# Performance work log

Measured on AMD Instinct MI355X. Metric: run time of the kernel, lower is better.

The kernel has to match this reference:

```python
import jax, jax.numpy as jnp
import numpy as np

N, C, H, W = 4, 256, 64, 64
K, G, PAD, STRIDE, DIL = 3, 8, 1, 1, 1
GC = C // G      # channels per group
P = K * K        # sampling points per group
HIN, WIN = H + 2 * PAD, W + 2 * PAD
BN_EPS = 1e-5
LN_EPS = 1e-5


def setup_inputs():
    key = jax.random.key(0)
    ks = jax.random.split(key, 8)
    f32 = jnp.float32
    return {
        "x": jax.random.normal(ks[0], (N, C, H, W), dtype=f32),
        "w_in": jax.random.normal(ks[1], (C, C), dtype=f32) * 0.05,
        "b_in": jnp.zeros((C,), f32),
        "w_dw": jax.random.normal(ks[2], (C, 1, K, K), dtype=f32) * 0.1,
        "b_dw": jnp.zeros((C,), f32),
        "ln_g": jnp.ones((C,), f32), "ln_b": jnp.zeros((C,), f32),
        "w_off": jax.random.normal(ks[3], (C, G * P * 2), dtype=f32) * 0.01,
        "b_off": jax.random.normal(ks[4], (G * P * 2,), dtype=f32) * 0.01,
        "w_mask": jax.random.normal(ks[5], (C, G * P), dtype=f32) * 0.01,
        "b_mask": jnp.zeros((G * P,), f32),
        "w_out": jax.random.normal(ks[6], (C, C), dtype=f32) * 0.05,
        "b_out": jnp.zeros((C,), f32),
        "bn_g": jnp.ones((C,), f32), "bn_b": jnp.zeros((C,), f32),
        "bn_mean": jnp.zeros((C,), f32), "bn_var": jnp.ones((C,), f32),
    }


def _bilinear(img, grid):
    # img: (B, Cc, Hh, Ww); grid: (B, S, P, 2) normalized to [-1,1],
    # matches F.grid_sample(mode='bilinear', padding_mode='zeros', align_corners=False)
    B, Cc, Hh, Ww = img.shape
    gx = (grid[..., 0] + 1.0) * 0.5 * Ww - 0.5
    gy = (grid[..., 1] + 1.0) * 0.5 * Hh - 0.5
    x0 = jnp.floor(gx)
    y0 = jnp.floor(gy)
    wx = gx - x0
    wy = gy - y0
    flat = img.reshape(B, Cc, Hh * Ww)

    def tap(xi, yi, wgt):
        valid = (xi >= 0) & (xi <= Ww - 1) & (yi >= 0) & (yi <= Hh - 1)
        idx = (jnp.clip(yi, 0, Hh - 1) * Ww + jnp.clip(xi, 0, Ww - 1)).astype(jnp.int32)
        v = jax.vmap(lambda im, ix: im[:, ix])(flat, idx)   # (B, Cc, S, P)
        return v * (wgt * valid.astype(img.dtype))[:, None]

    return (tap(x0, y0, (1 - wx) * (1 - wy)) + tap(x0 + 1, y0, wx * (1 - wy))
            + tap(x0, y0 + 1, (1 - wx) * wy) + tap(x0 + 1, y0 + 1, wx * wy))


def _forward(x, w_in, b_in, w_dw, b_dw, ln_g, ln_b, w_off, b_off,
             w_mask, b_mask, w_out, b_out, bn_g, bn_b, bn_mean, bn_var):
    xl = jnp.transpose(x, (0, 2, 3, 1))                      # (N,H,W,C) channels-last
    x_proj = xl @ w_in + b_in                                # input_proj
    # depthwise conv + LayerNorm + GELU feature branch for offset/mask prediction
    dw = jax.lax.conv_general_dilated(
        x, w_dw, (1, 1), ((PAD, PAD), (PAD, PAD)),
        feature_group_count=C, dimension_numbers=("NCHW", "OIHW", "NCHW"))
    dw = jnp.transpose(dw + b_dw[None, :, None, None], (0, 2, 3, 1))
    mu = dw.mean(-1, keepdims=True)
    var = ((dw - mu) ** 2).mean(-1, keepdims=True)
    dw = (dw - mu) * jax.lax.rsqrt(var + LN_EPS) * ln_g + ln_b
    x1 = jax.nn.gelu(dw, approximate=False)
    offset = x1 @ w_off + b_off                              # (N,H,W,G*P*2)
    mask = jax.nn.softmax((x1 @ w_mask + b_mask).reshape(N, H, W, G, P), axis=-1)
    # reference points + dilation kernel grid, normalized to padded input, (x,y) order
    ry = ((DIL * (K - 1)) // 2 + 0.5 + jnp.arange(H, dtype=x.dtype) * STRIDE) / HIN
    rx = ((DIL * (K - 1)) // 2 + 0.5 + jnp.arange(W, dtype=x.dtype) * STRIDE) / WIN
    ref = jnp.stack(jnp.broadcast_arrays(rx[None, :], ry[:, None]), axis=-1)  # (H,W,2)
    px = (jnp.arange(K, dtype=x.dtype) * DIL - (DIL * (K - 1)) // 2) / WIN
    py = (jnp.arange(K, dtype=x.dtype) * DIL - (DIL * (K - 1)) // 2) / HIN
    gx, gy = jnp.meshgrid(px, py, indexing="ij")             # kw-major flattening as in DCNv3
    kgrid = jnp.stack([gx, gy], -1).reshape(P, 2)
    norm = jnp.array([WIN, HIN], dtype=x.dtype)
    loc = (ref[None, :, :, None, None, :] + kgrid[None, None, None, None, :, :]
           + offset.reshape(N, H, W, G, P, 2) / norm)        # (N,H,W,G,P,2), offset_scale=1
    sgrid = 2.0 * loc - 1.0
    # group-split padded value tensor and deformable sampling
    xp = jnp.pad(x_proj, ((0, 0), (PAD, PAD), (PAD, PAD), (0, 0)))
    img = jnp.transpose(xp, (0, 3, 1, 2)).reshape(N * G, GC, HIN, WIN)
    sg = jnp.transpose(sgrid.reshape(N, H * W, G, P, 2), (0, 2, 1, 3, 4)).reshape(N * G, H * W, P, 2)
    sampled = _bilinear(img, sg)                             # (N*G, GC, H*W, P)
    m = jnp.transpose(mask.reshape(N, H * W, G, P), (0, 2, 1, 3)).reshape(N * G, 1, H * W, P)
    agg = (sampled * m).sum(-1)                              # (N*G, GC, H*W)
    y = jnp.transpose(agg.reshape(N, C, H * W), (0, 2, 1)).reshape(N, H, W, C)
    y = y @ w_out + b_out                                    # output_proj
    y = jnp.transpose(y, (0, 3, 1, 2))                       # back to NCHW
    y = (y - bn_mean[None, :, None, None]) * jax.lax.rsqrt(bn_var + BN_EPS)[None, :, None, None]
    y = y * bn_g[None, :, None, None] + bn_b[None, :, None, None]
    return y * jax.nn.sigmoid(y)                             # SiLU (Conv.default_act)


def reference(x, w_in, b_in, w_dw, b_dw, ln_g, ln_b, w_off, b_off,
              w_mask, b_mask, w_out, b_out, bn_g, bn_b, bn_mean, bn_var):
    return _forward(x, w_in, b_in, w_dw, b_dw, ln_g, ln_b, w_off, b_off,
                    w_mask, b_mask, w_out, b_out, bn_g, bn_b, bn_mean, bn_var)
```

## Files before the change

kernel.cpp:

```cpp
#include <hip/hip_runtime.h>
#include <math.h>

#define NB   4
#define CCH  256
#define HH   64
#define WW   64
#define GG   8
#define GCH  32
#define PP   9
#define HIN  66
#define WIN  66
#define HWSZ 4096
#define NPIX 16384

#define X16_ELEMS  (NPIX*CCH)
#define XP_ELEMS   (NB*HIN*WIN*CCH)
#define X1_ELEMS   (NPIX*CCH)
#define AGG_ELEMS  (NPIX*CCH)
#define WINT_ELEMS (CCH*CCH)
#define WOUTT_ELEMS (CCH*CCH)
#define WOMT_ELEMS (216*CCH)
#define OFF_ELEMS  (NPIX*144)
#define MSK_ELEMS  (NPIX*72)

typedef __attribute__((ext_vector_type(8))) short bf16x8;
typedef __attribute__((ext_vector_type(4))) float f32x4;

__device__ __forceinline__ unsigned short f2bf(float f) {
    unsigned int u = __float_as_uint(f);
    unsigned int r = (u + 0x7FFFu + ((u >> 16) & 1u)) >> 16;
    return (unsigned short)r;
}
__device__ __forceinline__ float bf2f(unsigned short s) {
    return __uint_as_float(((unsigned int)s) << 16);
}

#define SDW_STRIDE 258

__global__ __launch_bounds__(512) void k_dw_prep(
    const float* __restrict__ x, const float* __restrict__ w_dw,
    const float* __restrict__ b_dw, const float* __restrict__ ln_g,
    const float* __restrict__ ln_b, const float* __restrict__ w_in,
    const float* __restrict__ w_off, const float* __restrict__ w_mask,
    const float* __restrict__ w_out, unsigned short* __restrict__ x1,
    unsigned short* __restrict__ x16, unsigned short* __restrict__ win_t,
    unsigned short* __restrict__ womt, unsigned short* __restrict__ wout_t,
    unsigned short* __restrict__ xp)
{
    const int b = blockIdx.x;
    const int tid = threadIdx.x;

    if (b >= 256) {
        const int gtid = (b - 256) * 512 + tid;
        const int STRIDE = 68 * 512;
        for (int i = gtid; i < 252928; i += STRIDE) {
            if (i < 65536) {
                int n = i & 255, k = i >> 8;
                win_t[n * 256 + k] = f2bf(w_in[i]);
            } else if (i < 131072) {
                int j = i - 65536;
                int n = j & 255, k = j >> 8;
                wout_t[n * 256 + k] = f2bf(w_out[j]);
            } else if (i < 186368) {
                int j = i - 131072;
                int k = j / 216, col = j - k * 216;
                float v = (col < 144) ? w_off[k * 144 + col]
                                      : w_mask[k * 72 + col - 144];
                womt[col * 256 + k] = f2bf(v);
            } else {
                int r = i - 186368;
                int seg = r >> 6, ln = r & 63;
                int n = seg / 260, rp = seg % 260;
                int h, w;
                if (rp < 66)       { h = 0;        w = rp; }
                else if (rp < 132) { h = 65;       w = rp - 66; }
                else if (rp < 196) { h = rp - 131; w = 0; }
                else               { h = rp - 195; w = 65; }
                uint2 z = make_uint2(0u, 0u);
                *(uint2*)&xp[(((size_t)n * HIN + h) * WIN + w) * CCH + ln * 4] = z;
            }
        }
        return;
    }

    __shared__ unsigned short sdw[64 * SDW_STRIDE];
    __shared__ unsigned short sxr[64 * SDW_STRIDE];
    __shared__ float r1s[8][64];
    __shared__ float r2s[8][64];
    __shared__ float mu_s[64];
    __shared__ float rs_s[64];

    const int h = b & 63;
    const int n = b >> 6;
    const int wave = tid >> 6;
    const int lane = tid & 63;

    const float* xn = x + (size_t)n * CCH * HWSZ;
    const bool h0ok = (h > 0);
    const bool h2ok = (h < HH - 1);

    float s1 = 0.f, s2 = 0.f;

#pragma unroll 4
    for (int it = 0; it < 32; it++) {
        const int c = it * 8 + wave;
        const float* xc = xn + (size_t)c * HWSZ + h * WW + lane;
        float v0 = h0ok ? xc[-WW] : 0.f;
        float v1 = xc[0];
        float v2 = h2ok ? xc[WW] : 0.f;

        const float* wk = w_dw + c * 9;
        float acc = b_dw[c];

        float l0 = __shfl_up(v0, 1);   if (lane == 0)  l0 = 0.f;
        float r0 = __shfl_down(v0, 1); if (lane == 63) r0 = 0.f;
        acc += wk[0] * l0 + wk[1] * v0 + wk[2] * r0;

        float l1 = __shfl_up(v1, 1);   if (lane == 0)  l1 = 0.f;
        float r1 = __shfl_down(v1, 1); if (lane == 63) r1 = 0.f;
        acc += wk[3] * l1 + wk[4] * v1 + wk[5] * r1;

        float l2 = __shfl_up(v2, 1);   if (lane == 0)  l2 = 0.f;
        float r2 = __shfl_down(v2, 1); if (lane == 63) r2 = 0.f;
        acc += wk[6] * l2 + wk[7] * v2 + wk[8] * r2;

        s1 += acc;
        s2 += acc * acc;
        sdw[lane * SDW_STRIDE + c] = f2bf(acc);
        sxr[lane * SDW_STRIDE + c] = f2bf(v1);
    }

    r1s[wave][lane] = s1;
    r2s[wave][lane] = s2;
    __syncthreads();

    if (tid < 64) {
        float a1 = 0.f, a2 = 0.f;
#pragma unroll
        for (int q = 0; q < 8; q++) { a1 += r1s[q][tid]; a2 += r2s[q][tid]; }
        float mu = a1 * (1.0f / 256.0f);
        float var = a2 * (1.0f / 256.0f) - mu * mu;
        mu_s[tid] = mu;
        rs_s[tid] = rsqrtf(var + 1e-5f);
    }
    __syncthreads();

    const int c0 = (tid & 63) * 4;
    const int wq = tid >> 6;
    float g4[4], b4[4];
#pragma unroll
    for (int i = 0; i < 4; i++) { g4[i] = ln_g[c0 + i]; b4[i] = ln_b[c0 + i]; }

    unsigned short* x1p  = x1  + (((size_t)n * HH + h) * WW) * CCH + c0;
    unsigned short* x16p = x16 + (((size_t)n * HH + h) * WW) * CCH + c0;
#pragma unroll
    for (int pass = 0; pass < 8; pass++) {
        int w = wq + pass * 8;
        float mu = mu_s[w], rs = rs_s[w];
        const unsigned short* row  = &sdw[w * SDW_STRIDE + c0];
        const unsigned short* rowx = &sxr[w * SDW_STRIDE + c0];
        unsigned short tmp[4];
#pragma unroll
        for (int i = 0; i < 4; i++) {
            float v = (bf2f(row[i]) - mu) * rs * g4[i] + b4[i];
            tmp[i] = f2bf(0.5f * v * (1.0f + erff(v * 0.70710678118654752f)));
        }
        ushort4 o; o.x = tmp[0]; o.y = tmp[1]; o.z = tmp[2]; o.w = tmp[3];
        *(ushort4*)&x1p[(size_t)w * CCH] = o;
        ushort4 xo; xo.x = rowx[0]; xo.y = rowx[1]; xo.z = rowx[2]; xo.w = rowx[3];
        *(ushort4*)&x16p[(size_t)w * CCH] = xo;
    }
}

__global__ __launch_bounds__(256) void k_proj(
    const unsigned short* __restrict__ x16, const unsigned short* __restrict__ win_t,
    const float* __restrict__ b_in, unsigned short* __restrict__ xp,
    const unsigned short* __restrict__ x1, const unsigned short* __restrict__ womt,
    const float* __restrict__ b_off, const float* __restrict__ b_mask,
    float* __restrict__ off, float* __restrict__ msk)
{
    const int b = blockIdx.x;
    const int tid = threadIdx.x;
    const int wave = tid >> 6;
    const int lane = tid & 63;
    const int r16  = lane & 15;
    const int quad = lane >> 4;
    const int mw   = wave * 32;

    f32x4 acc[2][4];
#pragma unroll
    for (int i = 0; i < 2; i++)
#pragma unroll
        for (int j = 0; j < 4; j++) acc[i][j] = (f32x4){0.f, 0.f, 0.f, 0.f};

    if (b < 512) {
        const int m0  = (b & 127) * 128;
        const int co0 = (b >> 7) * 64;
        const int n   = m0 >> 12;
        const int hw0 = m0 & 4095;

        const unsigned short* a0p = x16 + (size_t)(m0 + mw + r16) * CCH + quad * 8;
        const unsigned short* a1p = a0p + 16 * CCH;

#pragma unroll
        for (int k0 = 0; k0 < CCH; k0 += 32) {
            bf16x8 a0 = *(const bf16x8*)&a0p[k0];
            bf16x8 a1 = *(const bf16x8*)&a1p[k0];
#pragma unroll
            for (int nt = 0; nt < 4; nt++) {
                bf16x8 bfr = *(const bf16x8*)&win_t[(size_t)(co0 + nt * 16 + r16) * CCH + k0 + quad * 8];
                acc[0][nt] = __builtin_amdgcn_mfma_f32_16x16x32_bf16(a0, bfr, acc[0][nt], 0, 0, 0);
                acc[1][nt] = __builtin_amdgcn_mfma_f32_16x16x32_bf16(a1, bfr, acc[1][nt], 0, 0, 0);
            }
        }

#pragma unroll
        for (int nt = 0; nt < 4; nt++) {
            int co = co0 + nt * 16 + r16;
            float bias = b_in[co];
#pragma unroll
            for (int mt = 0; mt < 2; mt++) {
                int mbase = mw + mt * 16 + quad * 4;
#pragma unroll
                for (int r = 0; r < 4; r++) {
                    int hw = hw0 + mbase + r;
                    int h = hw >> 6, w = hw & 63;
                    xp[(((size_t)n * HIN + (h + 1)) * WIN + (w + 1)) * CCH + co] =
                        f2bf(acc[mt][nt][r] + bias);
                }
            }
        }
    } else {
        const int b2 = b - 512;
        const int m0  = (b2 & 127) * 128;
        const int co0 = (b2 >> 7) * 64;

        const unsigned short* a0p = x1 + (size_t)(m0 + mw + r16) * CCH + quad * 8;
        const unsigned short* a1p = a0p + 16 * CCH;

#pragma unroll
        for (int k0 = 0; k0 < CCH; k0 += 32) {
            bf16x8 a0 = *(const bf16x8*)&a0p[k0];
            bf16x8 a1 = *(const bf16x8*)&a1p[k0];
#pragma unroll
            for (int nt = 0; nt < 4; nt++) {
                int col = co0 + nt * 16 + r16;
                int colc = (col < 216) ? col : 215;
                bf16x8 bfr = *(const bf16x8*)&womt[(size_t)colc * CCH + k0 + quad * 8];
                acc[0][nt] = __builtin_amdgcn_mfma_f32_16x16x32_bf16(a0, bfr, acc[0][nt], 0, 0, 0);
                acc[1][nt] = __builtin_amdgcn_mfma_f32_16x16x32_bf16(a1, bfr, acc[1][nt], 0, 0, 0);
            }
        }

#pragma unroll
        for (int nt = 0; nt < 4; nt++) {
            int col = co0 + nt * 16 + r16;
            if (col >= 216) continue;
            float bias = (col < 144) ? b_off[col] : b_mask[col - 144];
#pragma unroll
            for (int mt = 0; mt < 2; mt++) {
                int mbase = m0 + mw + mt * 16 + quad * 4;
#pragma unroll
                for (int r = 0; r < 4; r++) {
                    int p = mbase + r;
                    float v = acc[mt][nt][r] + bias;
                    if (col < 144) off[(size_t)p * 144 + col] = v;
                    else           msk[(size_t)p * 72 + col - 144] = v;
                }
            }
        }
    }
}

__device__ __forceinline__ void acc8_tap(float* a, uint4 vv, float wgt) {
    a[0] += wgt * __uint_as_float(vv.x << 16);
    a[1] += wgt * __uint_as_float(vv.x & 0xffff0000u);
    a[2] += wgt * __uint_as_float(vv.y << 16);
    a[3] += wgt * __uint_as_float(vv.y & 0xffff0000u);
    a[4] += wgt * __uint_as_float(vv.z << 16);
    a[5] += wgt * __uint_as_float(vv.z & 0xffff0000u);
    a[6] += wgt * __uint_as_float(vv.w << 16);
    a[7] += wgt * __uint_as_float(vv.w & 0xffff0000u);
}

__global__ __launch_bounds__(256) void k_sample_agg(
    const unsigned short* __restrict__ xp, const float* __restrict__ off,
    const float* __restrict__ msk, unsigned short* __restrict__ agg)
{
    __shared__ float  sm[576];
    __shared__ int2   tco[576];
    __shared__ float4 twt[576];

    const int tid = threadIdx.x;
    const int s0 = blockIdx.x * 8;

    if (tid < 64) {
        const int pix = tid >> 3, g = tid & 7;
        const float* mskp = msk + (size_t)(s0 + pix) * 72 + g * 9;
        float e[9];
        float mx = -1e30f;
#pragma unroll
        for (int p = 0; p < PP; p++) { e[p] = mskp[p]; mx = fmaxf(mx, e[p]); }
        float sum = 0.f;
#pragma unroll
        for (int p = 0; p < PP; p++) { e[p] = __expf(e[p] - mx); sum += e[p]; }
        float rs = 1.0f / sum;
#pragma unroll
        for (int p = 0; p < PP; p++) sm[tid * 9 + p] = e[p] * rs;
    }
    __syncthreads();

    for (int idx = tid; idx < 576; idx += 256) {
        int pix = idx / 72;
        int rem = idx - pix * 72;
        int g = rem / 9;
        int p = rem - g * 9;
        int s = s0 + pix;
        int hw = s & 4095;
        int h = hw >> 6, w = hw & 63;
        const float* offp = off + (size_t)s * 144 + g * 18 + p * 2;
        float ox = offp[0], oy = offp[1];
        int i = p / 3, j = p - i * 3;
        float fx = (float)(w + i) + ox;
        float fy = (float)(h + j) + oy;
        float x0f = floorf(fx), y0f = floorf(fy);
        int x0 = (int)x0f, y0 = (int)y0f;
        float wx = fx - x0f, wy = fy - y0f;
        float m = sm[idx];
        float w00 = (1.f - wx) * (1.f - wy) * m;
        float w10 = wx * (1.f - wy) * m;
        float w01 = (1.f - wx) * wy * m;
        float w11 = wx * wy * m;
        int x1c = x0 + 1, y1c = y0 + 1;
        if (!((x0  >= 0) && (x0  < WIN))) { w00 = 0.f; w01 = 0.f; }
        if (!((x1c >= 0) && (x1c < WIN))) { w10 = 0.f; w11 = 0.f; }
        if (!((y0  >= 0) && (y0  < HIN))) { w00 = 0.f; w10 = 0.f; }
        if (!((y1c >= 0) && (y1c < HIN))) { w01 = 0.f; w11 = 0.f; }
        int cx0 = min(max(x0, 0), WIN - 1), cx1 = min(max(x1c, 0), WIN - 1);
        int cy0 = min(max(y0, 0), HIN - 1), cy1 = min(max(y1c, 0), HIN - 1);
        tco[idx] = make_int2(cx0 | (cx1 << 16), cy0 | (cy1 << 16));
        twt[idx] = make_float4(w00, w10, w01, w11);
    }
    __syncthreads();

    const int pix = tid >> 5;
    const int l5 = tid & 31;
    const int g = l5 >> 2, c8 = l5 & 3;
    const int s = s0 + pix;
    const int n = s >> 12;
    const unsigned short* base = xp + (size_t)n * HIN * WIN * CCH + g * GCH + c8 * 8;
    const int tbase = pix * 72 + g * 9;

    float a[8];
#pragma unroll
    for (int i = 0; i < 8; i++) a[i] = 0.f;

#pragma unroll
    for (int p = 0; p < PP; p++) {
        int2 cc = tco[tbase + p];
        float4 wt = twt[tbase + p];
        int cx0 = cc.x & 0xFFFF, cx1 = cc.x >> 16;
        int cy0 = cc.y & 0xFFFF, cy1 = cc.y >> 16;
        const unsigned short* r0 = base + (size_t)(cy0 * WIN) * CCH;
        const unsigned short* r1 = base + (size_t)(cy1 * WIN) * CCH;
        uint4 v00 = *(const uint4*)&r0[(size_t)cx0 * CCH];
        uint4 v10 = *(const uint4*)&r0[(size_t)cx1 * CCH];
        uint4 v01 = *(const uint4*)&r1[(size_t)cx0 * CCH];
        uint4 v11 = *(const uint4*)&r1[(size_t)cx1 * CCH];
        acc8_tap(a, v00, wt.x);
        acc8_tap(a, v10, wt.y);
        acc8_tap(a, v01, wt.z);
        acc8_tap(a, v11, wt.w);
    }

    uint4 o;
    o.x = (unsigned int)f2bf(a[0]) | ((unsigned int)f2bf(a[1]) << 16);
    o.y = (unsigned int)f2bf(a[2]) | ((unsigned int)f2bf(a[3]) << 16);
    o.z = (unsigned int)f2bf(a[4]) | ((unsigned int)f2bf(a[5]) << 16);
    o.w = (unsigned int)f2bf(a[6]) | ((unsigned int)f2bf(a[7]) << 16);
    *(uint4*)&agg[(size_t)s * CCH + g * GCH + c8 * 8] = o;
}

__global__ __launch_bounds__(256) void k_gemm_out(
    const unsigned short* __restrict__ agg, const unsigned short* __restrict__ wout_t,
    const float* __restrict__ b_out, const float* __restrict__ bn_g,
    const float* __restrict__ bn_b, const float* __restrict__ bn_mean,
    const float* __restrict__ bn_var, float* __restrict__ out)
{
    const int m0  = blockIdx.x * 128;
    const int co0 = blockIdx.y * 64;
    const int tid = threadIdx.x;
    const int n   = m0 >> 12;
    const int hw0 = m0 & 4095;

    const int wave = tid >> 6;
    const int lane = tid & 63;
    const int r16  = lane & 15;
    const int quad = lane >> 4;
    const int mw   = wave * 32;

    f32x4 acc[2][4];
#pragma unroll
    for (int i = 0; i < 2; i++)
#pragma unroll
        for (int j = 0; j < 4; j++) acc[i][j] = (f32x4){0.f, 0.f, 0.f, 0.f};

    const unsigned short* a0p = agg + (size_t)(m0 + mw + r16) * CCH + quad * 8;
    const unsigned short* a1p = a0p + 16 * CCH;

#pragma unroll
    for (int k0 = 0; k0 < CCH; k0 += 32) {
        bf16x8 a0 = *(const bf16x8*)&a0p[k0];
        bf16x8 a1 = *(const bf16x8*)&a1p[k0];
#pragma unroll
        for (int nt = 0; nt < 4; nt++) {
            bf16x8 bfr = *(const bf16x8*)&wout_t[(size_t)(co0 + nt * 16 + r16) * CCH + k0 + quad * 8];
            acc[0][nt] = __builtin_amdgcn_mfma_f32_16x16x32_bf16(a0, bfr, acc[0][nt], 0, 0, 0);
            acc[1][nt] = __builtin_amdgcn_mfma_f32_16x16x32_bf16(a1, bfr, acc[1][nt], 0, 0, 0);
        }
    }

#pragma unroll
    for (int nt = 0; nt < 4; nt++) {
        int co = co0 + nt * 16 + r16;
        float mean = bn_mean[co];
        float rstd = rsqrtf(bn_var[co] + 1e-5f);
        float gg = bn_g[co], bb = bn_b[co], bo = b_out[co];
#pragma unroll
        for (int mt = 0; mt < 2; mt++) {
            int hwb = hw0 + mw + mt * 16 + quad * 4;
            float tmp[4];
#pragma unroll
            for (int r = 0; r < 4; r++) {
                float y = acc[mt][nt][r] + bo;
                float yh = (y - mean) * rstd * gg + bb;
                tmp[r] = yh / (1.0f + __expf(-yh));
            }
            float4 v = make_float4(tmp[0], tmp[1], tmp[2], tmp[3]);
            *(float4*)&out[((size_t)n * CCH + co) * HWSZ + hwb] = v;
        }
    }
}

extern "C" void kernel_launch(void* const* d_in, const int* in_sizes, int n_in,
                              void* d_out, int out_size, void* d_ws, size_t ws_size,
                              hipStream_t stream)
{
    const float* x       = (const float*)d_in[0];
    const float* w_in    = (const float*)d_in[1];
    const float* b_in    = (const float*)d_in[2];
    const float* w_dw    = (const float*)d_in[3];
    const float* b_dw    = (const float*)d_in[4];
    const float* ln_g    = (const float*)d_in[5];
    const float* ln_b    = (const float*)d_in[6];
    const float* w_off   = (const float*)d_in[7];
    const float* b_off   = (const float*)d_in[8];
    const float* w_mask  = (const float*)d_in[9];
    const float* b_mask  = (const float*)d_in[10];
    const float* w_out   = (const float*)d_in[11];
    const float* b_out   = (const float*)d_in[12];
    const float* bn_g    = (const float*)d_in[13];
    const float* bn_b    = (const float*)d_in[14];
    const float* bn_mean = (const float*)d_in[15];
    const float* bn_var  = (const float*)d_in[16];
    float* out = (float*)d_out;

    unsigned short* xp     = (unsigned short*)d_ws;
    unsigned short* x16    = xp + XP_ELEMS;
    unsigned short* x1     = x16 + X16_ELEMS;
    unsigned short* agg    = x1 + X1_ELEMS;
    unsigned short* win_t  = agg + AGG_ELEMS;
    unsigned short* wout_t = win_t + WINT_ELEMS;
    unsigned short* womt   = wout_t + WOUTT_ELEMS;
    float* off = (float*)(womt + WOMT_ELEMS);
    float* msk = off + OFF_ELEMS;

    k_dw_prep<<<dim3(324), 512, 0, stream>>>(x, w_dw, b_dw, ln_g, ln_b,
                                             w_in, w_off, w_mask, w_out,
                                             x1, x16, win_t, womt, wout_t, xp);
    k_proj<<<dim3(1024), 256, 0, stream>>>(x16, win_t, b_in, xp,
                                           x1, womt, b_off, b_mask, off, msk);
    k_sample_agg<<<dim3(2048), 256, 0, stream>>>(xp, off, msk, agg);
    k_gemm_out<<<dim3(128, 4), 256, 0, stream>>>(agg, wout_t, b_out, bn_g, bn_b, bn_mean, bn_var, out);
}
```

Before: 179.2 us.

## Fuse four stage kernels into one cooperative persistent kernel with grid syncs

Merges the depthwise/LN prep, input and offset/mask projections, deformable sampling and output GEMM into a single cooperative kernel of 512 blocks separated by grid.sync(). Each block now does several work items in sequence, and the dw prep moves from 512 to 256 threads per block. The aim is to remove launch gaps and kernel-boundary drains between stages. The cost is less parallelism per stage, 68KB of static shared memory limiting occupancy, and grid-wide barrier overhead. If the cooperative launch fails, it falls back to separate kernels.

```diff
diff --git a/kernel.cpp b/kernel.cpp
--- a/kernel.cpp
+++ b/kernel.cpp
@@ -1,5 +1,8 @@
 #include <hip/hip_runtime.h>
+#include <hip/hip_cooperative_groups.h>
 #include <math.h>
+
+namespace cg = cooperative_groups;
 
 #define NB   4
 #define CCH  256
@@ -37,61 +40,21 @@
 
 #define SDW_STRIDE 258
 
-__global__ __launch_bounds__(512) void k_dw_prep(
-    const float* __restrict__ x, const float* __restrict__ w_dw,
-    const float* __restrict__ b_dw, const float* __restrict__ ln_g,
-    const float* __restrict__ ln_b, const float* __restrict__ w_in,
-    const float* __restrict__ w_off, const float* __restrict__ w_mask,
-    const float* __restrict__ w_out, unsigned short* __restrict__ x1,
-    unsigned short* __restrict__ x16, unsigned short* __restrict__ win_t,
-    unsigned short* __restrict__ womt, unsigned short* __restrict__ wout_t,
-    unsigned short* __restrict__ xp)
-{
-    const int b = blockIdx.x;
-    const int tid = threadIdx.x;
-
-    if (b >= 256) {
-        const int gtid = (b - 256) * 512 + tid;
-        const int STRIDE = 68 * 512;
-        for (int i = gtid; i < 252928; i += STRIDE) {
-            if (i < 65536) {
-                int n = i & 255, k = i >> 8;
-                win_t[n * 256 + k] = f2bf(w_in[i]);
-            } else if (i < 131072) {
-                int j = i - 65536;
-                int n = j & 255, k = j >> 8;
-                wout_t[n * 256 + k] = f2bf(w_out[j]);
-            } else if (i < 186368) {
-                int j = i - 131072;
-                int k = j / 216, col = j - k * 216;
-                float v = (col < 144) ? w_off[k * 144 + col]
-                                      : w_mask[k * 72 + col - 144];
-                womt[col * 256 + k] = f2bf(v);
-            } else {
-                int r = i - 186368;
-                int seg = r >> 6, ln = r & 63;
-                int n = seg / 260, rp = seg % 260;
-                int h, w;
-                if (rp < 66)       { h = 0;        w = rp; }
-                else if (rp < 132) { h = 65;       w = rp - 66; }
-                else if (rp < 196) { h = rp - 131; w = 0; }
-                else               { h = rp - 195; w = 65; }
-                uint2 z = make_uint2(0u, 0u);
-                *(uint2*)&xp[(((size_t)n * HIN + h) * WIN + w) * CCH + ln * 4] = z;
-            }
-        }
-        return;
-    }
-
-    __shared__ unsigned short sdw[64 * SDW_STRIDE];
-    __shared__ unsigned short sxr[64 * SDW_STRIDE];
-    __shared__ float r1s[8][64];
-    __shared__ float r2s[8][64];
-    __shared__ float mu_s[64];
-    __shared__ float rs_s[64];
-
-    const int h = b & 63;
-    const int n = b >> 6;
+__device__ void dev_dw_row(int row, int tid, unsigned char* smem,
+                           const float* __restrict__ x, const float* __restrict__ w_dw,
+                           const float* __restrict__ b_dw, const float* __restrict__ ln_g,
+                           const float* __restrict__ ln_b, unsigned short* __restrict__ x1,
+                           unsigned short* __restrict__ x16)
+{
+    unsigned short* sdw = (unsigned short*)smem;
+    unsigned short* sxr = sdw + 64 * SDW_STRIDE;
+    float* r1s  = (float*)(smem + 66048);
+    float* r2s  = (float*)(smem + 67072);
+    float* mu_s = (float*)(smem + 68096);
+    float* rs_s = (float*)(smem + 68352);
+
+    const int h = row & 63;
+    const int n = row >> 6;
     const int wave = tid >> 6;
     const int lane = tid & 63;
 
@@ -102,8 +65,8 @@
     float s1 = 0.f, s2 = 0.f;
 
 #pragma unroll 4
-    for (int it = 0; it < 32; it++) {
-        const int c = it * 8 + wave;
+    for (int it = 0; it < 64; it++) {
+        const int c = it * 4 + wave;
         const float* xc = xn + (size_t)c * HWSZ + h * WW + lane;
         float v0 = h0ok ? xc[-WW] : 0.f;
         float v1 = xc[0];
@@ -130,14 +93,14 @@
         sxr[lane * SDW_STRIDE + c] = f2bf(v1);
     }
 
-    r1s[wave][lane] = s1;
-    r2s[wave][lane] = s2;
+    r1s[wave * 64 + lane] = s1;
+    r2s[wave * 64 + lane] = s2;
     __syncthreads();
 
     if (tid < 64) {
         float a1 = 0.f, a2 = 0.f;
 #pragma unroll
-        for (int q = 0; q < 8; q++) { a1 += r1s[q][tid]; a2 += r2s[q][tid]; }
+        for (int q = 0; q < 4; q++) { a1 += r1s[q * 64 + tid]; a2 += r2s[q * 64 + tid]; }
         float mu = a1 * (1.0f / 256.0f);
         float var = a2 * (1.0f / 256.0f) - mu * mu;
         mu_s[tid] = mu;
@@ -154,33 +117,69 @@
     unsigned short* x1p  = x1  + (((size_t)n * HH + h) * WW) * CCH + c0;
     unsigned short* x16p = x16 + (((size_t)n * HH + h) * WW) * CCH + c0;
 #pragma unroll
-    for (int pass = 0; pass < 8; pass++) {
-        int w = wq + pass * 8;
+    for (int pass = 0; pass < 16; pass++) {
+        int w = wq + pass * 4;
         float mu = mu_s[w], rs = rs_s[w];
-        const unsigned short* row  = &sdw[w * SDW_STRIDE + c0];
-        const unsigned short* rowx = &sxr[w * SDW_STRIDE + c0];
+        const unsigned short* row_c  = &sdw[w * SDW_STRIDE + c0];
+        const unsigned short* row_x  = &sxr[w * SDW_STRIDE + c0];
         unsigned short tmp[4];
 #pragma unroll
         for (int i = 0; i < 4; i++) {
-            float v = (bf2f(row[i]) - mu) * rs * g4[i] + b4[i];
+            float v = (bf2f(row_c[i]) - mu) * rs * g4[i] + b4[i];
             tmp[i] = f2bf(0.5f * v * (1.0f + erff(v * 0.70710678118654752f)));
         }
         ushort4 o; o.x = tmp[0]; o.y = tmp[1]; o.z = tmp[2]; o.w = tmp[3];
         *(ushort4*)&x1p[(size_t)w * CCH] = o;
-        ushort4 xo; xo.x = rowx[0]; xo.y = rowx[1]; xo.z = rowx[2]; xo.w = rowx[3];
+        ushort4 xo; xo.x = row_x[0]; xo.y = row_x[1]; xo.z = row_x[2]; xo.w = row_x[3];
         *(ushort4*)&x16p[(size_t)w * CCH] = xo;
     }
 }
 
-__global__ __launch_bounds__(256) void k_proj(
-    const unsigned short* __restrict__ x16, const unsigned short* __restrict__ win_t,
-    const float* __restrict__ b_in, unsigned short* __restrict__ xp,
-    const unsigned short* __restrict__ x1, const unsigned short* __restrict__ womt,
-    const float* __restrict__ b_off, const float* __restrict__ b_mask,
-    float* __restrict__ off, float* __restrict__ msk)
-{
-    const int b = blockIdx.x;
-    const int tid = threadIdx.x;
+__device__ void dev_misc(int gtid, int stride,
+                         const float* __restrict__ w_in, const float* __restrict__ w_off,
+                         const float* __restrict__ w_mask, const float* __restrict__ w_out,
+                         unsigned short* __restrict__ win_t, unsigned short* __restrict__ womt,
+                         unsigned short* __restrict__ wout_t, unsigned short* __restrict__ xp)
+{
+    for (int i = gtid; i < 252928; i += stride) {
+        if (i < 65536) {
+            int n = i & 255, k = i >> 8;
+            win_t[n * 256 + k] = f2bf(w_in[i]);
+        } else if (i < 131072) {
+            int j = i - 65536;
+            int n = j & 255, k = j >> 8;
+            wout_t[n * 256 + k] = f2bf(w_out[j]);
+        } else if (i < 186368) {
+            int j = i - 131072;
+            int k = j / 216, col = j - k * 216;
+            float v = (col < 144) ? w_off[k * 144 + col] : w_mask[k * 72 + col - 144];
+            womt[col * 256 + k] = f2bf(v);
+        } else {
+            int r = i - 186368;
+            int seg = r >> 6, ln = r & 63;
+            int n = seg / 260, rp = seg % 260;
+            int h, w;
+            if (rp < 66)       { h = 0;        w = rp; }
+            else if (rp < 132) { h = 65;       w = rp - 66; }
+            else if (rp < 196) { h = rp - 131; w = 0; }
+            else               { h = rp - 195; w = 65; }
+            uint2 z = make_uint2(0u, 0u);
+            *(uint2*)&xp[(((size_t)n * HIN + h) * WIN + w) * CCH + ln * 4] = z;
+        }
+    }
+}
+
+__device__ void dev_gemm_in_tile(int tile, int tid,
+                                 const unsigned short* __restrict__ x16,
+                                 const unsigned short* __restrict__ win_t,
+                                 const float* __restrict__ b_in,
+                                 unsigned short* __restrict__ xp)
+{
+    const int m0  = (tile & 127) * 128;
+    const int co0 = (tile >> 7) * 64;
+    const int n   = m0 >> 12;
+    const int hw0 = m0 & 4095;
+
     const int wave = tid >> 6;
     const int lane = tid & 63;
     const int r16  = lane & 15;
@@ -193,80 +192,92 @@
 #pragma unroll
         for (int j = 0; j < 4; j++) acc[i][j] = (f32x4){0.f, 0.f, 0.f, 0.f};
 
-    if (b < 512) {
-        const int m0  = (b & 127) * 128;
-        const int co0 = (b >> 7) * 64;
-        const int n   = m0 >> 12;
-        const int hw0 = m0 & 4095;
-
-        const unsigned short* a0p = x16 + (size_t)(m0 + mw + r16) * CCH + quad * 8;
-        const unsigned short* a1p = a0p + 16 * CCH;
-
-#pragma unroll
-        for (int k0 = 0; k0 < CCH; k0 += 32) {
-            bf16x8 a0 = *(const bf16x8*)&a0p[k0];
-            bf16x8 a1 = *(const bf16x8*)&a1p[k0];
-#pragma unroll
-            for (int nt = 0; nt < 4; nt++) {
-                bf16x8 bfr = *(const bf16x8*)&win_t[(size_t)(co0 + nt * 16 + r16) * CCH + k0 + quad * 8];
-                acc[0][nt] = __builtin_amdgcn_mfma_f32_16x16x32_bf16(a0, bfr, acc[0][nt], 0, 0, 0);
-                acc[1][nt] = __builtin_amdgcn_mfma_f32_16x16x32_bf16(a1, bfr, acc[1][nt], 0, 0, 0);
+    const unsigned short* a0p = x16 + (size_t)(m0 + mw + r16) * CCH + quad * 8;
+    const unsigned short* a1p = a0p + 16 * CCH;
+
+#pragma unroll
+    for (int k0 = 0; k0 < CCH; k0 += 32) {
+        bf16x8 a0 = *(const bf16x8*)&a0p[k0];
+        bf16x8 a1 = *(const bf16x8*)&a1p[k0];
+#pragma unroll
+        for (int nt = 0; nt < 4; nt++) {
+            bf16x8 bfr = *(const bf16x8*)&win_t[(size_t)(co0 + nt * 16 + r16) * CCH + k0 + quad * 8];
+            acc[0][nt] = __builtin_amdgcn_mfma_f32_16x16x32_bf16(a0, bfr, acc[0][nt], 0, 0, 0);
+            acc[1][nt] = __builtin_amdgcn_mfma_f32_16x16x32_bf16(a1, bfr, acc[1][nt], 0, 0, 0);
+        }
+    }
+
+#pragma unroll
+    for (int nt = 0; nt < 4; nt++) {
+        int co = co0 + nt * 16 + r16;
+        float bias = b_in[co];
+#pragma unroll
+        for (int mt = 0; mt < 2; mt++) {
+            int mbase = mw + mt * 16 + quad * 4;
+#pragma unroll
+            for (int r = 0; r < 4; r++) {
+                int hw = hw0 + mbase + r;
+                int h = hw >> 6, w = hw & 63;
+                xp[(((size_t)n * HIN + (h + 1)) * WIN + (w + 1)) * CCH + co] =
+                    f2bf(acc[mt][nt][r] + bias);
             }
         }
-
-#pragma unroll
-        for (int nt = 0; nt < 4; nt++) {
-            int co = co0 + nt * 16 + r16;
-            float bias = b_in[co];
-#pragma unroll
-            for (int mt = 0; mt < 2; mt++) {
-                int mbase = mw + mt * 16 + quad * 4;
-#pragma unroll
-                for (int r = 0; r < 4; r++) {
-                    int hw = hw0 + mbase + r;
-                    int h = hw >> 6, w = hw & 63;
-                    xp[(((size_t)n * HIN + (h + 1)) * WIN + (w + 1)) * CCH + co] =
-                        f2bf(acc[mt][nt][r] + bias);
-                }
-            }
-        }
-    } else {
-        const int b2 = b - 512;
-        const int m0  = (b2 & 127) * 128;
-        const int co0 = (b2 >> 7) * 64;
-
-        const unsigned short* a0p = x1 + (size_t)(m0 + mw + r16) * CCH + quad * 8;
-        const unsigned short* a1p = a0p + 16 * CCH;
-
-#pragma unroll
-        for (int k0 = 0; k0 < CCH; k0 += 32) {
-            bf16x8 a0 = *(const bf16x8*)&a0p[k0];
-            bf16x8 a1 = *(const bf16x8*)&a1p[k0];
-#pragma unroll
-            for (int nt = 0; nt < 4; nt++) {
-                int col = co0 + nt * 16 + r16;
-                int colc = (col < 216) ? col : 215;
-                bf16x8 bfr = *(const bf16x8*)&womt[(size_t)colc * CCH + k0 + quad * 8];
-                acc[0][nt] = __builtin_amdgcn_mfma_f32_16x16x32_bf16(a0, bfr, acc[0][nt], 0, 0, 0);
-                acc[1][nt] = __builtin_amdgcn_mfma_f32_16x16x32_bf16(a1, bfr, acc[1][nt], 0, 0, 0);
-            }
-        }
-
+    }
+}
+
+__device__ void dev_offmask_tile(int tile, int tid,
+                                 const unsigned short* __restrict__ x1,
+                                 const unsigned short* __restrict__ womt,
+                                 const float* __restrict__ b_off,
+                                 const float* __restrict__ b_mask,
+                                 float* __restrict__ off, float* __restrict__ msk)
+{
+    const int m0  = (tile & 127) * 128;
+    const int co0 = (tile >> 7) * 64;
+
+    const int wave = tid >> 6;
+    const int lane = tid & 63;
+    const int r16  = lane & 15;
+    const int quad = lane >> 4;
+    const int mw   = wave * 32;
+
+    f32x4 acc[2][4];
+#pragma unroll
+    for (int i = 0; i < 2; i++)
+#pragma unroll
+        for (int j = 0; j < 4; j++) acc[i][j] = (f32x4){0.f, 0.f, 0.f, 0.f};
+
+    const unsigned short* a0p = x1 + (size_t)(m0 + mw + r16) * CCH + quad * 8;
+    const unsigned short* a1p = a0p + 16 * CCH;
+
+#pragma unroll
+    for (int k0 = 0; k0 < CCH; k0 += 32) {
+        bf16x8 a0 = *(const bf16x8*)&a0p[k0];
+        bf16x8 a1 = *(const bf16x8*)&a1p[k0];
 #pragma unroll
         for (int nt = 0; nt < 4; nt++) {
             int col = co0 + nt * 16 + r16;
-            if (col >= 216) continue;
-            float bias = (col < 144) ? b_off[col] : b_mask[col - 144];
-#pragma unroll
-            for (int mt = 0; mt < 2; mt++) {
-                int mbase = m0 + mw + mt * 16 + quad * 4;
-#pragma unroll
-                for (int r = 0; r < 4; r++) {
-                    int p = mbase + r;
-                    float v = acc[mt][nt][r] + bias;
-                    if (col < 144) off[(size_t)p * 144 + col] = v;
-                    else           msk[(size_t)p * 72 + col - 144] = v;
-                }
+            int colc = (col < 216) ? col : 215;
+            bf16x8 bfr = *(const bf16x8*)&womt[(size_t)colc * CCH + k0 + quad * 8];
+            acc[0][nt] = __builtin_amdgcn_mfma_f32_16x16x32_bf16(a0, bfr, acc[0][nt], 0, 0, 0);
+            acc[1][nt] = __builtin_amdgcn_mfma_f32_16x16x32_bf16(a1, bfr, acc[1][nt], 0, 0, 0);
+        }
+    }
+
+#pragma unroll
+    for (int nt = 0; nt < 4; nt++) {
+        int col = co0 + nt * 16 + r16;
+        if (col >= 216) continue;
+        float bias = (col < 144) ? b_off[col] : b_mask[col - 144];
+#pragma unroll
+        for (int mt = 0; mt < 2; mt++) {
+            int mbase = m0 + mw + mt * 16 + quad * 4;
+#pragma unroll
+            for (int r = 0; r < 4; r++) {
+                int p = mbase + r;
+                float v = acc[mt][nt][r] + bias;
+                if (col < 144) off[(size_t)p * 144 + col] = v;
+                else           msk[(size_t)p * 72 + col - 144] = v;
             }
         }
     }
@@ -283,16 +294,14 @@
     a[7] += wgt * __uint_as_float(vv.w & 0xffff0000u);
 }
 
-__global__ __launch_bounds__(256) void k_sample_agg(
-    const unsigned short* __restrict__ xp, const float* __restrict__ off,
-    const float* __restrict__ msk, unsigned short* __restrict__ agg)
-{
-    __shared__ float  sm[576];
-    __shared__ int2   tco[576];
-    __shared__ float4 twt[576];
-
-    const int tid = threadIdx.x;
-    const int s0 = blockIdx.x * 8;
+__device__ void dev_sample8(int s0, int tid, unsigned char* smem,
+                            const unsigned short* __restrict__ xp,
+                            const float* __restrict__ off, const float* __restrict__ msk,
+                            unsigned short* __restrict__ agg)
+{
+    float*  sm  = (float*)smem;
+    int2*   tco = (int2*)(smem + 2304);
+    float4* twt = (float4*)(smem + 6912);
 
     if (tid < 64) {
         const int pix = tid >> 3, g = tid & 7;
@@ -381,15 +390,15 @@
     *(uint4*)&agg[(size_t)s * CCH + g * GCH + c8 * 8] = o;
 }
 
-__global__ __launch_bounds__(256) void k_gemm_out(
-    const unsigned short* __restrict__ agg, const unsigned short* __restrict__ wout_t,
-    const float* __restrict__ b_out, const float* __restrict__ bn_g,
-    const float* __restrict__ bn_b, const float* __restrict__ bn_mean,
-    const float* __restrict__ bn_var, float* __restrict__ out)
-{
-    const int m0  = blockIdx.x * 128;
-    const int co0 = blockIdx.y * 64;
-    const int tid = threadIdx.x;
+__device__ void dev_out_tile(int tile, int tid,
+                             const unsigned short* __restrict__ agg,
+                             const unsigned short* __restrict__ wout_t,
+                             const float* __restrict__ b_out, const float* __restrict__ bn_g,
+                             const float* __restrict__ bn_b, const float* __restrict__ bn_mean,
+                             const float* __restrict__ bn_var, float* __restrict__ out)
+{
+    const int m0  = (tile & 127) * 128;
+    const int co0 = (tile >> 7) * 64;
     const int n   = m0 >> 12;
     const int hw0 = m0 & 4095;
 
@@ -440,6 +449,81 @@
             *(float4*)&out[((size_t)n * CCH + co) * HWSZ + hwb] = v;
         }
     }
+}
+
+__global__ __launch_bounds__(256, 2) void k_mega(
+    const float* x, const float* w_in, const float* b_in, const float* w_dw,
+    const float* b_dw, const float* ln_g, const float* ln_b, const float* w_off,
+    const float* b_off, const float* w_mask, const float* b_mask, const float* w_out,
+    const float* b_out, const float* bn_g, const float* bn_b, const float* bn_mean,
+    const float* bn_var, float* out,
+    unsigned short* xp, unsigned short* x16, unsigned short* x1, unsigned short* agg,
+    unsigned short* win_t, unsigned short* womt, unsigned short* wout_t,
+    float* off, float* msk)
+{
+    __shared__ __align__(16) unsigned char smem[68608];
+    cg::grid_group grid = cg::this_grid();
+    const int b = blockIdx.x;
+    const int tid = threadIdx.x;
+
+    if (b < 256) {
+        dev_dw_row(b, tid, smem, x, w_dw, b_dw, ln_g, ln_b, x1, x16);
+    } else {
+        dev_misc((b - 256) * 256 + tid, 256 * 256,
+                 w_in, w_off, w_mask, w_out, win_t, womt, wout_t, xp);
+    }
+    grid.sync();
+
+    dev_gemm_in_tile(b, tid, x16, win_t, b_in, xp);
+    dev_offmask_tile(b, tid, x1, womt, b_off, b_mask, off, msk);
+    grid.sync();
+
+    for (int rep = 0; rep < 4; rep++) {
+        __syncthreads();
+        dev_sample8((b * 4 + rep) * 8, tid, smem, xp, off, msk, agg);
+    }
+    grid.sync();
+
+    dev_out_tile(b, tid, agg, wout_t, b_out, bn_g, bn_b, bn_mean, bn_var, out);
+}
+
+__global__ __launch_bounds__(256) void k_dw_prep_f(
+    const float* x, const float* w_dw, const float* b_dw, const float* ln_g,
+    const float* ln_b, const float* w_in, const float* w_off, const float* w_mask,
+    const float* w_out, unsigned short* x1, unsigned short* x16,
+    unsigned short* win_t, unsigned short* womt, unsigned short* wout_t,
+    unsigned short* xp)
+{
+    __shared__ __align__(16) unsigned char smem[68608];
+    const int b = blockIdx.x, tid = threadIdx.x;
+    if (b < 256) dev_dw_row(b, tid, smem, x, w_dw, b_dw, ln_g, ln_b, x1, x16);
+    else dev_misc((b - 256) * 256 + tid, 68 * 256,
+                  w_in, w_off, w_mask, w_out, win_t, womt, wout_t, xp);
+}
+
+__global__ __launch_bounds__(256) void k_proj_f(
+    const unsigned short* x16, const unsigned short* win_t, const float* b_in,
+    unsigned short* xp, const unsigned short* x1, const unsigned short* womt,
+    const float* b_off, const float* b_mask, float* off, float* msk)
+{
+    const int b = blockIdx.x, tid = threadIdx.x;
+    if (b < 512) dev_gemm_in_tile(b, tid, x16, win_t, b_in, xp);
+    else         dev_offmask_tile(b - 512, tid, x1, womt, b_off, b_mask, off, msk);
+}
+
+__global__ __launch_bounds__(256) void k_sample_f(
+    const unsigned short* xp, const float* off, const float* msk, unsigned short* agg)
+{
+    __shared__ __align__(16) unsigned char smem[16128];
+    dev_sample8(blockIdx.x * 8, threadIdx.x, smem, xp, off, msk, agg);
+}
+
+__global__ __launch_bounds__(256) void k_out_f(
+    const unsigned short* agg, const unsigned short* wout_t, const float* b_out,
+    const float* bn_g, const float* bn_b, const float* bn_mean,
+    const float* bn_var, float* out)
+{
+    dev_out_tile(blockIdx.x, threadIdx.x, agg, wout_t, b_out, bn_g, bn_b, bn_mean, bn_var, out);
 }
 
 extern "C" void kernel_launch(void* const* d_in, const int* in_sizes, int n_in,
@@ -475,11 +559,25 @@
     float* off = (float*)(womt + WOMT_ELEMS);
     float* msk = off + OFF_ELEMS;
 
-    k_dw_prep<<<dim3(324), 512, 0, stream>>>(x, w_dw, b_dw, ln_g, ln_b,
-                                             w_in, w_off, w_mask, w_out,
-                                             x1, x16, win_t, womt, wout_t, xp);
-    k_proj<<<dim3(1024), 256, 0, stream>>>(x16, win_t, b_in, xp,
-                                           x1, womt, b_off, b_mask, off, msk);
-    k_sample_agg<<<dim3(2048), 256, 0, stream>>>(xp, off, msk, agg);
-    k_gemm_out<<<dim3(128, 4), 256, 0, stream>>>(agg, wout_t, b_out, bn_g, bn_b, bn_mean, bn_var, out);
-}
+    void* args[] = {
+        (void*)&x, (void*)&w_in, (void*)&b_in, (void*)&w_dw, (void*)&b_dw,
+        (void*)&ln_g, (void*)&ln_b, (void*)&w_off, (void*)&b_off, (void*)&w_mask,
+        (void*)&b_mask, (void*)&w_out, (void*)&b_out, (void*)&bn_g, (void*)&bn_b,
+        (void*)&bn_mean, (void*)&bn_var, (void*)&out,
+        (void*)&xp, (void*)&x16, (void*)&x1, (void*)&agg,
+        (void*)&win_t, (void*)&womt, (void*)&wout_t, (void*)&off, (void*)&msk
+    };
+
+    hipError_t err = hipLaunchCooperativeKernel((const void*)k_mega, dim3(512), dim3(256),
+                                                args, 0, stream);
+    if (err != hipSuccess) {
+        k_dw_prep_f<<<dim3(324), 256, 0, stream>>>(x, w_dw, b_dw, ln_g, ln_b,
+                                                   w_in, w_off, w_mask, w_out,
+                                                   x1, x16, win_t, womt, wout_t, xp);
+        k_proj_f<<<dim3(1024), 256, 0, stream>>>(x16, win_t, b_in, xp,
+                                                 x1, womt, b_off, b_mask, off, msk);
+        k_sample_f<<<dim3(2048), 256, 0, stream>>>(xp, off, msk, agg);
+        k_out_f<<<dim3(512), 256, 0, stream>>>(agg, wout_t, b_out,
+                                               bn_g, bn_b, bn_mean, bn_var, out);
+    }
+}
```

Measured after the change: 421.1 us. 135% more time.
